# Kernel tuning notes

Measured on AMD Instinct MI355X. Metric: run time of the kernel, lower is better.

Reference implementation:

```python
import jax, jax.numpy as jnp
import numpy as np

P = 7  # output_size


def _axis_weights(start, length, dim):
    """Per-roi 1D interpolation matrix A [R, P, dim] such that the roi_align
    output separates as out = Ay @ fm @ Ax^T (torchvision roi_align,
    aligned=False, sampling_ratio=-1 i.e. adaptive ceil(bin) samples)."""
    S = int(np.ceil(dim / P))  # max samples per bin (rois lie inside the image)
    bin_sz = length / P                               # [R]
    grid = jnp.ceil(length / P).astype(jnp.int32)     # adaptive samples per bin, [R]
    g = grid.astype(jnp.float32)[:, None, None]       # [R,1,1]
    s = jnp.arange(S, dtype=jnp.float32)              # [S]
    ph = jnp.arange(P, dtype=jnp.float32)             # [P]
    # sample coordinate: start + ph*bin + (s+0.5)*bin/grid  -> [R,P,S]
    coord = (start[:, None, None] + ph[None, :, None] * bin_sz[:, None, None]
             + (s[None, None, :] + 0.5) * bin_sz[:, None, None] / g)
    valid = (coord >= -1.0) & (coord <= dim)
    c = jnp.maximum(coord, 0.0)
    low = jnp.floor(c).astype(jnp.int32)
    hi_clamp = low >= dim - 1
    low = jnp.where(hi_clamp, dim - 1, low)
    high = jnp.where(hi_clamp, dim - 1, low + 1)
    cv = jnp.where(hi_clamp, low.astype(jnp.float32), c)
    l = cv - low.astype(jnp.float32)
    smask = (s[None, None, :] < g) & valid            # mask unused samples
    w = smask.astype(jnp.float32) / g                 # 1/count split per axis
    w_low = (1.0 - l) * w
    w_high = l * w
    R = start.shape[0]
    r_idx = jnp.arange(R)[:, None, None]
    p_idx = jnp.arange(P)[None, :, None]
    A = jnp.zeros((R, P, dim), dtype=jnp.float32)
    A = A.at[r_idx, p_idx, low].add(w_low)
    A = A.at[r_idx, p_idx, high].add(w_high)
    return A


def _roi_align(fm, rois):
    # fm: [C,H,W]; rois: [R,4] = (x1,y1,x2,y2); spatial_scale=1.0
    C, H, W = fm.shape
    x1, y1, x2, y2 = rois[:, 0], rois[:, 1], rois[:, 2], rois[:, 3]
    roi_w = jnp.maximum(x2 - x1, 1.0)
    roi_h = jnp.maximum(y2 - y1, 1.0)
    Ay = _axis_weights(y1, roi_h, H)                  # [R,P,H]
    Ax = _axis_weights(x1, roi_w, W)                  # [R,P,W]
    tmp = jnp.einsum('rph,chw->rcpw', Ay, fm)         # [R,C,P,W]
    return jnp.einsum('rcpw,rqw->rcpq', tmp, Ax)      # [R,C,P,P]


def _per_image(fm, b, g):
    # fm: [C,H,W], b: [N,4] boxes, g: [M,4] gt boxes
    N, M = b.shape[0], g.shape[0]
    # context boxes: union (min of mins, max of maxes) of every (box, gt) pair
    x1 = jnp.minimum(b[:, None, 0], g[None, :, 0])
    y1 = jnp.minimum(b[:, None, 1], g[None, :, 1])
    x2 = jnp.maximum(b[:, None, 2], g[None, :, 2])
    y2 = jnp.maximum(b[:, None, 3], g[None, :, 3])
    ctx = jnp.stack([x1, y1, x2, y2], axis=-1).reshape(N * M, 4)
    feats = _roi_align(fm, jnp.concatenate([b, ctx], axis=0))  # [N+N*M,C,P,P]
    box_f = feats[:N]
    ctx_mean = feats[N:].reshape(N, M, feats.shape[1], P, P).mean(axis=1)
    return box_f + ctx_mean                            # [N,C,P,P]


def setup_inputs() -> dict:
    key = jax.random.key(0)
    B, C, H, W, N, M = 2, 256, 56, 56, 64, 8
    k1, k2, k3, k4, k5 = jax.random.split(key, 5)
    feature_map = jax.random.normal(k1, (B, C, H, W), dtype=jnp.float32)
    # boxes inside the feature map, max side 0.35*H so adaptive grid <= ceil(H/7)
    b_xy1 = jax.random.uniform(k2, (B, N, 2), minval=0.0, maxval=0.64 * H)
    b_wh = jax.random.uniform(k3, (B, N, 2), minval=4.0, maxval=0.35 * H)
    boxes = jnp.concatenate([b_xy1, b_xy1 + b_wh], axis=-1).astype(jnp.float32)
    g_xy1 = jax.random.uniform(k4, (B, M, 2), minval=0.0, maxval=0.64 * H)
    g_wh = jax.random.uniform(k5, (B, M, 2), minval=4.0, maxval=0.35 * H)
    gt_boxes = jnp.concatenate([g_xy1, g_xy1 + g_wh], axis=-1).astype(jnp.float32)
    return {"feature_map": feature_map, "boxes": boxes, "gt_boxes": gt_boxes}


def reference(feature_map, boxes, gt_boxes):
    # returns [B, N, C, P, P] (stacked version of the per-image list output)
    return jax.vmap(_per_image)(feature_map, boxes, gt_boxes)
```

## Files before the change

### kernel.cpp

```cpp
#include <hip/hip_runtime.h>

#define B_ 2
#define C_ 256
#define H_ 56
#define W_ 56
#define N_ 64
#define M_ 8
#define P_ 7
#define Y2_ (H_/2)
#define Y4_ (H_/4)
#define SCTX_ 4
#define JPN_ (1 + (M_)*SCTX_)
#define JP2_ (9*4)
#define WROW_ 8

typedef _Float16 half2v __attribute__((ext_vector_type(2)));

#if __has_builtin(__builtin_amdgcn_fdot2)
#define FDOT2(a, b, c) __builtin_amdgcn_fdot2((a), (b), (c), false)
#else
static __device__ __forceinline__ float FDOT2(half2v a, half2v b, float c) {
    return fmaf((float)a.x, (float)b.x, fmaf((float)a.y, (float)b.y, c));
}
#endif

#define F_FMT4 0
#define N_FMT4 (B_*Y4_*W_*C_*2)
#define F_OUTS (F_FMT4 + N_FMT4)
#define N_OUTS (B_*N_*49*C_)
#define WS_BYTES_F ((size_t)(F_OUTS + N_OUTS) * 4)
#define F_PART (F_FMT4 + N_FMT4)
#define N_PART (B_*N_*7*9*7*C_)
#define WS_BYTES_P ((size_t)(F_PART + N_PART) * 4)

#define PREP_T (B_*Y4_*4*2)
#define PREP_N (PREP_T + 784)

__global__ __launch_bounds__(256) void k_prep(const float* __restrict__ fm,
                                              float* __restrict__ ws_f) {
    __shared__ float t[28 * 257 + 8];
    int bid = blockIdx.x;
    int tid = (int)threadIdx.x;

    if (bid < PREP_T) {
        int xh = bid & 1;
        int cg = (bid >> 1) & 3;
        int y4 = (bid >> 3) % Y4_;
        int b  = (bid >> 3) / Y4_;
        int c0 = cg * 64, x0 = xh * 28;
        for (int e = tid; e < 64 * 4 * 28; e += 256) {
            int c_l = e / 112, rem = e % 112;
            int y_l = rem / 28, x_l = rem % 28;
            t[x_l * 257 + y_l * 64 + c_l] =
                fm[(((size_t)b * C_ + c0 + c_l) * H_ + 4 * y4 + y_l) * W_ + x0 + x_l];
        }
        __syncthreads();
        uint2* dst = (uint2*)ws_f;
        for (int e = tid; e < 28 * 64; e += 256) {
            int x_l = e >> 6, c_l = e & 63;
            const float* p = &t[x_l * 257 + c_l];
            half2v lo, hi; uint2 o;
            lo.x = (_Float16)p[0];   lo.y = (_Float16)p[64];
            hi.x = (_Float16)p[128]; hi.y = (_Float16)p[192];
            o.x = __builtin_bit_cast(unsigned int, lo);
            o.y = __builtin_bit_cast(unsigned int, hi);
            dst[(((size_t)b * Y4_ + y4) * W_ + x0 + x_l) * (size_t)C_ + c0 + c_l] = o;
        }
        return;
    }

    {
        int tz = (bid - PREP_T) * 256 + tid;
        float4 z = {0.0f, 0.0f, 0.0f, 0.0f};
        float4* dst = (float4*)(ws_f + F_OUTS);
        dst[tz * 2]     = z;
        dst[tz * 2 + 1] = z;
    }
}

static __device__ __forceinline__ void gen_weights(int k, int b, int n, int tid,
                                                   const float* __restrict__ boxes,
                                                   const float* __restrict__ gt,
                                                   float (*s_wyf)[WROW_],
                                                   unsigned int* s_wy2,
                                                   float (*s_ax)[WROW_],
                                                   float& bx1, float& by1,
                                                   float& rw, float& rh) {
    const float* bp = boxes + ((size_t)b * N_ + n) * 4;
    float bx2, by2;
    if (k == 0) {
        bx1 = bp[0]; by1 = bp[1]; bx2 = bp[2]; by2 = bp[3];
    } else {
        const float* gp = gt + ((size_t)b * M_ + (k - 1)) * 4;
        bx1 = fminf(bp[0], gp[0]); by1 = fminf(bp[1], gp[1]);
        bx2 = fmaxf(bp[2], gp[2]); by2 = fmaxf(bp[3], gp[3]);
    }
    rw = fmaxf(bx2 - bx1, 1.0f);
    rh = fmaxf(by2 - by1, 1.0f);

    for (int e = tid; e < H_ * WROW_; e += 256) ((float*)s_wyf)[e] = 0.0f;
    for (int e = tid; e < W_ * WROW_; e += 256) ((float*)s_ax)[e] = 0.0f;
    __syncthreads();

    if (tid < P_) {
        int p = tid;
        float bin = rh / 7.0f;
        float gf  = ceilf(bin);
        int   g   = (int)gf;
        float ivg = 1.0f / gf;
        float start = by1 + (float)p * bin;
        for (int ss = 0; ss < g; ++ss) {
            float coord = start + ((float)ss + 0.5f) * bin * ivg;
            if (coord < -1.0f || coord > (float)H_) continue;
            float cc = fmaxf(coord, 0.0f);
            int low = (int)floorf(cc);
            int high; float l;
            if (low >= H_ - 1) { low = H_ - 1; high = H_ - 1; l = 0.0f; }
            else               { high = low + 1; l = cc - (float)low; }
            s_wyf[low][p]  += (1.0f - l) * ivg;
            s_wyf[high][p] += l * ivg;
        }
    } else if (tid >= 64 && tid < 64 + P_) {
        int p = tid - 64;
        float bin = rw / 7.0f;
        float gf  = ceilf(bin);
        int   g   = (int)gf;
        float ivg = 1.0f / gf;
        float fs  = (k == 0) ? ivg : ivg * (1.0f / (float)M_);
        float start = bx1 + (float)p * bin;
        for (int ss = 0; ss < g; ++ss) {
            float coord = start + ((float)ss + 0.5f) * bin * ivg;
            if (coord < -1.0f || coord > (float)W_) continue;
            float cc = fmaxf(coord, 0.0f);
            int low = (int)floorf(cc);
            int high; float l;
            if (low >= W_ - 1) { low = W_ - 1; high = W_ - 1; l = 0.0f; }
            else               { high = low + 1; l = cc - (float)low; }
            s_ax[low][p]  += (1.0f - l) * fs;
            s_ax[high][p] += l * fs;
        }
    }
    __syncthreads();

    if (tid < Y2_ * WROW_) {
        int q2 = tid >> 3, col = tid & 7;
        half2v h;
        if (col < P_) { h.x = (_Float16)s_wyf[2 * q2][col]; h.y = (_Float16)s_wyf[2 * q2 + 1][col]; }
        else          { h.x = (_Float16)0.0f; h.y = (_Float16)0.0f; }
        s_wy2[tid] = __builtin_bit_cast(unsigned int, h);
    }
    __syncthreads();
}

#define YQ3(F) \
    { cs[0][F] = FDOT2(w1[F], v0b, FDOT2(w0[F], v0a, cs[0][F]));   \
      cs[1][F] = FDOT2(w1[F], v1b, FDOT2(w0[F], v1a, cs[1][F]));   \
      cs[2][F] = FDOT2(w1[F], v2b, FDOT2(w0[F], v2a, cs[2][F]));   \
      cs[3][F] = FDOT2(w1[F], v3b, FDOT2(w0[F], v3a, cs[3][F])); }

__global__ __launch_bounds__(256, 4) void k_mainP(const float* __restrict__ ws_f,
                                                  const float* __restrict__ boxes,
                                                  const float* __restrict__ gt,
                                                  float* __restrict__ part) {
    __shared__ float        s_wyf[H_][WROW_];
    __shared__ unsigned int s_wy2[Y2_ * WROW_];
    __shared__ float        s_ax[W_][WROW_];
    __shared__ int          s_lm[Y4_];

    int bid = blockIdx.x;
    int j   = bid % JP2_;
    int n   = (bid / JP2_) & (N_ - 1);
    int b   = bid / (JP2_ * N_);
    int k   = j >> 2;
    int s   = j & 3;
    int p0  = 2 * s;
    int tid = (int)threadIdx.x;
    int c   = tid;

    float bx1, by1, rw, rh;
    gen_weights(k, b, n, tid, boxes, gt, s_wyf, s_wy2, s_ax, bx1, by1, rw, rh);

    if (tid < Y4_) {
        int m = 0;
#pragma unroll
        for (int r = 0; r < 4; ++r)
#pragma unroll
            for (int p = 0; p < P_; ++p)
                if (s_wyf[4 * tid + r][p] != 0.0f) m |= 1 << p;
        s_lm[tid] = m;
    }
    __syncthreads();

    float binw = rw * (1.0f / 7.0f);
    float lo_f = bx1 + (float)p0 * binw;
    int   pe   = (p0 + 1 < P_) ? p0 + 2 : p0 + 1;
    float hi_f = bx1 + (float)pe * binw;
    int xs = min(max((int)floorf(fmaxf(lo_f, 0.0f)), 0), W_ - 1);
    int xe = min(max((int)floorf(fminf(hi_f, (float)W_)) + 1, 0), W_ - 1) + 1;

    int ylo = min(max((int)floorf(fmaxf(by1, 0.0f)), 0), H_ - 1);
    int yhi = min(max((int)floorf(by1 + rh) + 1, 0), H_ - 1) + 1;
    int ylo4 = ylo >> 2;
    int yhi4 = (yhi + 3) >> 2;

    const uint2* f4 = (const uint2*)ws_f + (size_t)b * (Y4_ * W_ * C_);

    float acc0[P_], acc1[P_];
#pragma unroll
    for (int q = 0; q < P_; ++q) { acc0[q] = 0.0f; acc1[q] = 0.0f; }

    if (xs < xe) {
        for (int x = xs; x < xe; x += 4) {
            float cs[4][P_];
#pragma unroll
            for (int i = 0; i < 4; ++i)
#pragma unroll
                for (int py = 0; py < P_; ++py) cs[i][py] = 0.0f;

            const uint2* cp = f4 + ((size_t)(ylo4 * W_ + x)) * C_ + c;
            for (int y4 = ylo4; y4 < yhi4; ++y4) {
                int lm = s_lm[y4];
                if (lm == 0) { cp += W_ * C_; continue; }
                uint2 d0 = cp[0];
                uint2 d1 = cp[C_];
                uint2 d2 = cp[2 * C_];
                uint2 d3 = cp[3 * C_];
                uint4 wa0 = *(const uint4*)&s_wy2[(2 * y4) * WROW_];
                uint4 wb0 = *(const uint4*)&s_wy2[(2 * y4) * WROW_ + 4];
                uint4 wa1 = *(const uint4*)&s_wy2[(2 * y4 + 1) * WROW_];
                uint4 wb1 = *(const uint4*)&s_wy2[(2 * y4 + 1) * WROW_ + 4];
                half2v w0[7], w1[7];
                w0[0] = __builtin_bit_cast(half2v, wa0.x);
                w0[1] = __builtin_bit_cast(half2v, wa0.y);
                w0[2] = __builtin_bit_cast(half2v, wa0.z);
                w0[3] = __builtin_bit_cast(half2v, wa0.w);
                w0[4] = __builtin_bit_cast(half2v, wb0.x);
                w0[5] = __builtin_bit_cast(half2v, wb0.y);
                w0[6] = __builtin_bit_cast(half2v, wb0.z);
                w1[0] = __builtin_bit_cast(half2v, wa1.x);
                w1[1] = __builtin_bit_cast(half2v, wa1.y);
                w1[2] = __builtin_bit_cast(half2v, wa1.z);
                w1[3] = __builtin_bit_cast(half2v, wa1.w);
                w1[4] = __builtin_bit_cast(half2v, wb1.x);
                w1[5] = __builtin_bit_cast(half2v, wb1.y);
                w1[6] = __builtin_bit_cast(half2v, wb1.z);
                half2v v0a = __builtin_bit_cast(half2v, d0.x);
                half2v v0b = __builtin_bit_cast(half2v, d0.y);
                half2v v1a = __builtin_bit_cast(half2v, d1.x);
                half2v v1b = __builtin_bit_cast(half2v, d1.y);
                half2v v2a = __builtin_bit_cast(half2v, d2.x);
                half2v v2b = __builtin_bit_cast(half2v, d2.y);
                half2v v3a = __builtin_bit_cast(half2v, d3.x);
                half2v v3b = __builtin_bit_cast(half2v, d3.y);

                if (lm & 0x01) YQ3(0)
                if (lm & 0x02) YQ3(1)
                if (lm & 0x04) YQ3(2)
                if (lm & 0x08) YQ3(3)
                if (lm & 0x10) YQ3(4)
                if (lm & 0x20) YQ3(5)
                if (lm & 0x40) YQ3(6)
                cp += W_ * C_;
            }

#pragma unroll
            for (int i = 0; i < 4; ++i) {
                if (x + i < xe) {
                    float2 axv = *(const float2*)&s_ax[x + i][p0];
#pragma unroll
                    for (int py = 0; py < P_; ++py) {
                        acc0[py] = fmaf(axv.x, cs[i][py], acc0[py]);
                        acc1[py] = fmaf(axv.y, cs[i][py], acc1[py]);
                    }
                }
            }
        }
    }

    size_t bn = (size_t)b * N_ + n;
    float* pp = part + (((bn * 7 + p0) * 9 + k) * 7) * 256 + c;
#pragma unroll
    for (int py = 0; py < P_; ++py) pp[py * 256] = acc0[py];
    if (p0 + 1 < P_) {
        float* pq = part + (((bn * 7 + p0 + 1) * 9 + k) * 7) * 256 + c;
#pragma unroll
        for (int py = 0; py < P_; ++py) pq[py * 256] = acc1[py];
    }
}

__global__ __launch_bounds__(256) void k_reduce(const float* __restrict__ part,
                                                float* __restrict__ out) {
    __shared__ float t[49 * 65];
    int bid = blockIdx.x;
    int cg  = bid & 3;
    int bn  = bid >> 2;
    int tid = (int)threadIdx.x;
    const float* pb = part + (size_t)bn * (7 * 9 * 7 * 256) + cg * 64;
    for (int e = tid; e < 49 * 64; e += 256) {
        int q = e >> 6, cl = e & 63;
        int py = q / 7, px = q - py * 7;
        const float* p0 = pb + ((size_t)(px * 63 + py)) * 256 + cl;
        float sum = 0.0f;
#pragma unroll
        for (int k = 0; k < 9; ++k) sum += p0[(size_t)k * (7 * 256)];
        t[q * 65 + cl] = sum;
    }
    __syncthreads();
    float* dst = out + (size_t)bn * (C_ * 49) + (size_t)cg * 64 * 49;
    for (int e = tid; e < 64 * 49; e += 256) {
        int cl = e / 49, q = e - cl * 49;
        dst[e] = t[q * 65 + cl];
    }
}

__global__ __launch_bounds__(256, 4) void k_main(const float* __restrict__ ws_f,
                                                 const float* __restrict__ boxes,
                                                 const float* __restrict__ gt,
                                                 float* __restrict__ outs) {
    __shared__ float        s_wyf[H_][WROW_];
    __shared__ unsigned int s_wy2[Y2_ * WROW_];
    __shared__ float        s_ax[W_][WROW_];

    int bid = blockIdx.x;
    int j   = bid % JPN_;
    int n   = (bid / JPN_) & (N_ - 1);
    int b   = bid / (JPN_ * N_);
    int k, s;
    if (j == 0) { k = 0; s = 0; }
    else        { k = 1 + ((j - 1) >> 2); s = (j - 1) & 3; }
    int tid = (int)threadIdx.x;
    int c   = tid;

    float bx1, by1, rw, rh;
    gen_weights(k, b, n, tid, boxes, gt, s_wyf, s_wy2, s_ax, bx1, by1, rw, rh);

    int xlo = min(max((int)floorf(fmaxf(bx1, 0.0f)), 0), W_ - 1);
    int xhi = min(max((int)floorf(bx1 + rw) + 1, 0), W_ - 1) + 1;
    int ylo = min(max((int)floorf(fmaxf(by1, 0.0f)), 0), H_ - 1);
    int yhi = min(max((int)floorf(by1 + rh) + 1, 0), H_ - 1) + 1;
    int xs, xe;
    if (k == 0) { xs = xlo; xe = xhi; }
    else {
        int cw = (xhi - xlo + SCTX_ - 1) >> 2;
        xs = xlo + s * cw;
        xe = min(xs + cw, xhi);
    }
    if (xs >= xe) return;

    int ylo4 = ylo >> 2;
    int yhi4 = (yhi + 3) >> 2;

    const uint2* f4 = (const uint2*)ws_f + (size_t)b * (Y4_ * W_ * C_);

    float acc[49];
#pragma unroll
    for (int q = 0; q < 49; ++q) acc[q] = 0.0f;
    int live = 0;

    for (int x = xs; x < xe; x += 4) {
        float cs[4][P_];
#pragma unroll
        for (int i = 0; i < 4; ++i)
#pragma unroll
            for (int py = 0; py < P_; ++py) cs[i][py] = 0.0f;

        const uint2* cp = f4 + ((size_t)(ylo4 * W_ + x)) * C_ + c;

        uint2 d0 = cp[0];
        uint2 d1 = cp[C_];
        uint2 d2 = cp[2 * C_];
        uint2 d3 = cp[3 * C_];
        for (int y4 = ylo4; y4 < yhi4; ++y4) {
            size_t nstep = (y4 + 1 < yhi4) ? (size_t)(W_ * C_) : 0;
            const uint2* cq = cp + nstep;
            uint2 e0 = cq[0];
            uint2 e1 = cq[C_];
            uint2 e2 = cq[2 * C_];
            uint2 e3 = cq[3 * C_];

            uint4 wa0 = *(const uint4*)&s_wy2[(2 * y4) * WROW_];
            uint4 wb0 = *(const uint4*)&s_wy2[(2 * y4) * WROW_ + 4];
            uint4 wa1 = *(const uint4*)&s_wy2[(2 * y4 + 1) * WROW_];
            uint4 wb1 = *(const uint4*)&s_wy2[(2 * y4 + 1) * WROW_ + 4];
            half2v w0[7], w1[7];
            w0[0] = __builtin_bit_cast(half2v, wa0.x);
            w0[1] = __builtin_bit_cast(half2v, wa0.y);
            w0[2] = __builtin_bit_cast(half2v, wa0.z);
            w0[3] = __builtin_bit_cast(half2v, wa0.w);
            w0[4] = __builtin_bit_cast(half2v, wb0.x);
            w0[5] = __builtin_bit_cast(half2v, wb0.y);
            w0[6] = __builtin_bit_cast(half2v, wb0.z);
            w1[0] = __builtin_bit_cast(half2v, wa1.x);
            w1[1] = __builtin_bit_cast(half2v, wa1.y);
            w1[2] = __builtin_bit_cast(half2v, wa1.z);
            w1[3] = __builtin_bit_cast(half2v, wa1.w);
            w1[4] = __builtin_bit_cast(half2v, wb1.x);
            w1[5] = __builtin_bit_cast(half2v, wb1.y);
            w1[6] = __builtin_bit_cast(half2v, wb1.z);
            half2v v0a = __builtin_bit_cast(half2v, d0.x);
            half2v v0b = __builtin_bit_cast(half2v, d0.y);
            half2v v1a = __builtin_bit_cast(half2v, d1.x);
            half2v v1b = __builtin_bit_cast(half2v, d1.y);
            half2v v2a = __builtin_bit_cast(half2v, d2.x);
            half2v v2b = __builtin_bit_cast(half2v, d2.y);
            half2v v3a = __builtin_bit_cast(half2v, d3.x);
            half2v v3b = __builtin_bit_cast(half2v, d3.y);
#pragma unroll
            for (int py = 0; py < P_; ++py) {
                cs[0][py] = FDOT2(w1[py], v0b, FDOT2(w0[py], v0a, cs[0][py]));
                cs[1][py] = FDOT2(w1[py], v1b, FDOT2(w0[py], v1a, cs[1][py]));
                cs[2][py] = FDOT2(w1[py], v2b, FDOT2(w0[py], v2a, cs[2][py]));
                cs[3][py] = FDOT2(w1[py], v3b, FDOT2(w0[py], v3a, cs[3][py]));
            }
            d0 = e0; d1 = e1; d2 = e2; d3 = e3;
            cp = cq;
        }

#pragma unroll
        for (int i = 0; i < 4; ++i) {
            if (x + i < xe) {
                float av[8];
                *(float4*)(&av[0]) = *(const float4*)&s_ax[x + i][0];
                *(float4*)(&av[4]) = *(const float4*)&s_ax[x + i][4];
#pragma unroll
                for (int px = 0; px < P_; ++px) {
                    float w = av[px];
                    if (w != 0.0f) {
                        live |= 1 << px;
#pragma unroll
                        for (int py = 0; py < P_; ++py)
                            acc[py * P_ + px] = fmaf(w, cs[i][py], acc[py * P_ + px]);
                    }
                }
            }
        }
    }

    float* os = outs + ((size_t)b * N_ + n) * (49 * C_) + c;
#pragma unroll
    for (int px = 0; px < P_; ++px) {
        if (live & (1 << px)) {
#pragma unroll
            for (int py = 0; py < P_; ++py)
                atomicAdd(os + (py * P_ + px) * C_, acc[py * P_ + px]);
        }
    }
}

__global__ __launch_bounds__(256) void k_final(const float* __restrict__ outs,
                                               float* __restrict__ out) {
    __shared__ float t[49 * 65];
    int bid = blockIdx.x;
    int cg  = bid & 3;
    int bn  = bid >> 2;
    int tid = (int)threadIdx.x;
    const float* src = outs + (size_t)bn * (49 * C_) + cg * 64;
    for (int e = tid; e < 49 * 64; e += 256) {
        int q = e >> 6, c = e & 63;
        t[q * 65 + c] = src[q * C_ + c];
    }
    __syncthreads();
    float* dst = out + (size_t)bn * (C_ * 49) + (size_t)cg * 64 * 49;
    for (int e = tid; e < 64 * 49; e += 256) {
        int c = e / 49, q = e - c * 49;
        dst[e] = t[q * 65 + c];
    }
}

extern "C" void kernel_launch(void* const* d_in, const int* in_sizes, int n_in,
                              void* d_out, int out_size, void* d_ws, size_t ws_size,
                              hipStream_t stream) {
    const float* fm    = (const float*)d_in[0];
    const float* boxes = (const float*)d_in[1];
    const float* gt    = (const float*)d_in[2];
    float* ws_f = (float*)d_ws;
    float* out  = (float*)d_out;

    if (ws_size >= WS_BYTES_P) {
        float* part = ws_f + F_PART;
        k_prep<<<PREP_T, 256, 0, stream>>>(fm, ws_f);
        k_mainP<<<B_ * N_ * JP2_, 256, 0, stream>>>(ws_f, boxes, gt, part);
        k_reduce<<<B_ * N_ * 4, 256, 0, stream>>>(part, out);
    } else {
        float* outs = ws_f + F_OUTS;
        k_prep<<<PREP_N, 256, 0, stream>>>(fm, ws_f);
        k_main<<<B_ * N_ * JPN_, 256, 0, stream>>>(ws_f, boxes, gt, outs);
        k_final<<<B_ * N_ * 4, 256, 0, stream>>>(outs, out);
    }
}
```

Baseline: 135.4 us.

## Remap mainP blocks across XCDs, split prep finer, vectorize reduce loads

Adds a dedicated prep kernel for the partial-sum path that uses 32-channel tiles, doubling the block count for better parallelism while producing the same fp16 packed layout. The main partial kernel now decodes its block index so that each image's work lands on a fixed subset of XCDs, aiming to improve L2 locality of the feature map. The reduce kernel loads float4 partials instead of scalar loads to cut memory instruction count. These are three independent tweaks, and the block remap assumes 8 XCDs with round-robin dispatch.

```diff
diff --git a/kernel.cpp b/kernel.cpp
--- a/kernel.cpp
+++ b/kernel.cpp
@@ -33,8 +33,39 @@
 #define N_PART (B_*N_*7*9*7*C_)
 #define WS_BYTES_P ((size_t)(F_PART + N_PART) * 4)
 
+#define PREPP_T (B_*Y4_*8*2)
 #define PREP_T (B_*Y4_*4*2)
 #define PREP_N (PREP_T + 784)
+
+__global__ __launch_bounds__(256) void k_prepP(const float* __restrict__ fm,
+                                               float* __restrict__ ws_f) {
+    __shared__ float t[28 * 129 + 8];
+    int bid = blockIdx.x;
+    int tid = (int)threadIdx.x;
+    int xh = bid & 1;
+    int cg = (bid >> 1) & 7;
+    int y4 = (bid >> 4) % Y4_;
+    int b  = (bid >> 4) / Y4_;
+    int c0 = cg * 32, x0 = xh * 28;
+    for (int e = tid; e < 32 * 4 * 28; e += 256) {
+        int c_l = e / 112, rem = e % 112;
+        int y_l = rem / 28, x_l = rem % 28;
+        t[x_l * 129 + y_l * 32 + c_l] =
+            fm[(((size_t)b * C_ + c0 + c_l) * H_ + 4 * y4 + y_l) * W_ + x0 + x_l];
+    }
+    __syncthreads();
+    uint2* dst = (uint2*)ws_f;
+    for (int e = tid; e < 28 * 32; e += 256) {
+        int x_l = e >> 5, c_l = e & 31;
+        const float* p = &t[x_l * 129 + c_l];
+        half2v lo, hi; uint2 o;
+        lo.x = (_Float16)p[0];  lo.y = (_Float16)p[32];
+        hi.x = (_Float16)p[64]; hi.y = (_Float16)p[96];
+        o.x = __builtin_bit_cast(unsigned int, lo);
+        o.y = __builtin_bit_cast(unsigned int, hi);
+        dst[(((size_t)b * Y4_ + y4) * W_ + x0 + x_l) * (size_t)C_ + c0 + c_l] = o;
+    }
+}
 
 __global__ __launch_bounds__(256) void k_prep(const float* __restrict__ fm,
                                               float* __restrict__ ws_f) {
@@ -167,15 +198,18 @@
     __shared__ float        s_ax[W_][WROW_];
     __shared__ int          s_lm[Y4_];
 
-    int bid = blockIdx.x;
-    int j   = bid % JP2_;
-    int n   = (bid / JP2_) & (N_ - 1);
-    int b   = bid / (JP2_ * N_);
-    int k   = j >> 2;
-    int s   = j & 3;
-    int p0  = 2 * s;
-    int tid = (int)threadIdx.x;
-    int c   = tid;
+    int bid0 = (int)blockIdx.x;
+    int xcd  = bid0 & 7;
+    int g    = bid0 >> 3;
+    int b    = xcd & 1;
+    int wj   = g * 4 + (xcd >> 1);
+    int j    = wj % JP2_;
+    int n    = wj / JP2_;
+    int k    = j >> 2;
+    int s    = j & 3;
+    int p0   = 2 * s;
+    int tid  = (int)threadIdx.x;
+    int c    = tid;
 
     float bx1, by1, rw, rh;
     gen_weights(k, b, n, tid, boxes, gt, s_wyf, s_wy2, s_ax, bx1, by1, rw, rh);
@@ -295,15 +329,19 @@
     int cg  = bid & 3;
     int bn  = bid >> 2;
     int tid = (int)threadIdx.x;
-    const float* pb = part + (size_t)bn * (7 * 9 * 7 * 256) + cg * 64;
-    for (int e = tid; e < 49 * 64; e += 256) {
-        int q = e >> 6, cl = e & 63;
+    const float4* pb4 = (const float4*)(part + (size_t)bn * (7 * 9 * 7 * 256) + cg * 64);
+    for (int e = tid; e < 49 * 16; e += 256) {
+        int q = e >> 4, c4 = e & 15;
         int py = q / 7, px = q - py * 7;
-        const float* p0 = pb + ((size_t)(px * 63 + py)) * 256 + cl;
-        float sum = 0.0f;
-#pragma unroll
-        for (int k = 0; k < 9; ++k) sum += p0[(size_t)k * (7 * 256)];
-        t[q * 65 + cl] = sum;
+        const float4* p0 = pb4 + (size_t)(px * 63 + py) * 64 + c4;
+        float4 sum = {0.0f, 0.0f, 0.0f, 0.0f};
+#pragma unroll
+        for (int k = 0; k < 9; ++k) {
+            float4 v = p0[(size_t)k * 448];
+            sum.x += v.x; sum.y += v.y; sum.z += v.z; sum.w += v.w;
+        }
+        float* tq = &t[q * 65 + c4 * 4];
+        tq[0] = sum.x; tq[1] = sum.y; tq[2] = sum.z; tq[3] = sum.w;
     }
     __syncthreads();
     float* dst = out + (size_t)bn * (C_ * 49) + (size_t)cg * 64 * 49;
@@ -478,7 +516,7 @@
 
     if (ws_size >= WS_BYTES_P) {
         float* part = ws_f + F_PART;
-        k_prep<<<PREP_T, 256, 0, stream>>>(fm, ws_f);
+        k_prepP<<<PREPP_T, 256, 0, stream>>>(fm, ws_f);
         k_mainP<<<B_ * N_ * JP2_, 256, 0, stream>>>(ws_f, boxes, gt, part);
         k_reduce<<<B_ * N_ * 4, 256, 0, stream>>>(part, out);
     } else {
```

New measurement: 132.1 us. 2.4% less time.
